# Performance work log

Hardware: AMD Instinct MI355X
Metric: run time of the kernel (lower is better)

Reference implementation:

```python
import jax, jax.numpy as jnp
import numpy as np


def setup_inputs() -> dict:
    key = jax.random.key(0)
    kx, kw = jax.random.split(key)
    x = jax.random.normal(kx, (4096, 4096), dtype=jnp.float32)
    weight = jax.random.uniform(kw, (7, 7), dtype=jnp.float32)
    bias = jnp.zeros((1,), dtype=jnp.float32)
    return {"x": x, "weight": weight, "bias": bias}


def reference(x, weight, bias):
    # Valid 2D cross-correlation (stride 1, no padding) + scalar bias,
    # identical math to corr2d(X, K) + bias in the torch module.
    lhs = x[None, None, :, :]          # [N=1, C=1, H, W]
    rhs = weight[None, None, :, :]     # [O=1, I=1, kh, kw]
    y = jax.lax.conv_general_dilated(
        lhs, rhs,
        window_strides=(1, 1),
        padding='VALID',
        dimension_numbers=('NCHW', 'OIHW', 'NCHW'),
    )
    return y[0, 0] + bias[0]  # [H-kh+1, W-kw+1]
```

## Files before the change

### kernel.cpp

```cpp
#include <hip/hip_runtime.h>

#define N   4096
#define ON  4090
#define LDS_W 136
#define CPR   34
#define WBUF  2048
#define GX  32
#define GY  512
#define NT  (GX * GY)
#define NB  (NT / 4)

__device__ __forceinline__ void gload_lds16(const float* g, float* l) {
    __builtin_amdgcn_global_load_lds(
        (const __attribute__((address_space(1))) void*)g,
        (__attribute__((address_space(3))) void*)l,
        16, 0, 0);
}

__global__ __launch_bounds__(256, 5)
void conv7x7_wave(const float* __restrict__ x,
                  const float* __restrict__ w,
                  const float* __restrict__ bias,
                  float* __restrict__ out)
{
    __shared__ float lds[4 * WBUF];

    const int tid  = threadIdx.x;
    const int lane = tid & 63;
    const int wv   = tid >> 6;
    float* buf = lds + (wv << 11);

    const int b  = blockIdx.x;
    const int bs = (b & 7) * (NB / 8) + (b >> 3);
    const int t  = (bs << 2) + wv;
    const int bx = t & (GX - 1);
    const int by = t >> 5;
    const int x0 = bx << 7;
    const int y0 = by << 3;

    {
        const int xc0 = x0 >> 2;
        #pragma unroll
        for (int k = 0; k < 8; ++k) {
            const int m   = (k << 6) + lane;
            const int row = m / CPR;
            const int cc  = m - row * CPR;
            const int gy  = min(y0 + row, N - 1);
            const int gc  = min(xc0 + cc, (N >> 2) - 1);
            const float* src = x + ((size_t)gy << 12) + ((size_t)gc << 2);
            gload_lds16(src, buf + (k << 8));
        }
    }

    float ws[49];
    #pragma unroll
    for (int i = 0; i < 49; ++i) ws[i] = w[i];
    const float bv = bias[0];

    asm volatile("s_waitcnt vmcnt(0)" ::: "memory");

    const int tau   = lane & 31;
    const int rg2   = lane >> 5;
    const int colf  = tau << 2;
    const int rbase = rg2 << 2;

    float acc[4][4] = {};

    #pragma unroll
    for (int rr = 0; rr < 10; ++rr) {
        const float* rp = buf + (rbase + rr) * LDS_W + colf;
        float v[10];
        const float4 a = *reinterpret_cast<const float4*>(rp);
        const float4 bq = *reinterpret_cast<const float4*>(rp + 4);
        const float2 c = *reinterpret_cast<const float2*>(rp + 8);
        v[0]=a.x;  v[1]=a.y;  v[2]=a.z;  v[3]=a.w;
        v[4]=bq.x; v[5]=bq.y; v[6]=bq.z; v[7]=bq.w;
        v[8]=c.x;  v[9]=c.y;

        #pragma unroll
        for (int r = 0; r < 4; ++r) {
            const int ky = rr - r;
            if (ky >= 0 && ky < 7) {
                #pragma unroll
                for (int kx = 0; kx < 7; ++kx) {
                    const float wk = ws[ky * 7 + kx];
                    #pragma unroll
                    for (int j = 0; j < 4; ++j)
                        acc[r][j] = fmaf(v[kx + j], wk, acc[r][j]);
                }
            }
        }
    }

    const int ox  = x0 + colf;
    const int oy0 = y0 + rbase;
    if (ox + 4 <= ON && oy0 + 4 <= ON) {
        #pragma unroll
        for (int r = 0; r < 4; ++r) {
            float* dst = out + (size_t)(oy0 + r) * ON + ox;
            *reinterpret_cast<float2*>(dst)     = make_float2(acc[r][0] + bv, acc[r][1] + bv);
            *reinterpret_cast<float2*>(dst + 2) = make_float2(acc[r][2] + bv, acc[r][3] + bv);
        }
    } else {
        #pragma unroll
        for (int r = 0; r < 4; ++r) {
            const int oy = oy0 + r;
            if (oy < ON) {
                float* dst = out + (size_t)oy * ON;
                #pragma unroll
                for (int j = 0; j < 4; ++j) {
                    const int oxj = ox + j;
                    if (oxj < ON) dst[oxj] = acc[r][j] + bv;
                }
            }
        }
    }
}

extern "C" void kernel_launch(void* const* d_in, const int* in_sizes, int n_in,
                              void* d_out, int out_size, void* d_ws, size_t ws_size,
                              hipStream_t stream) {
    const float* x    = (const float*)d_in[0];
    const float* w    = (const float*)d_in[1];
    const float* bias = (const float*)d_in[2];
    float* out        = (float*)d_out;

    conv7x7_wave<<<dim3(NB, 1, 1), dim3(256, 1, 1), 0, stream>>>(x, w, bias, out);
}
```

Baseline: 33.55 us.

## Double-buffer LDS staging so each wave processes four row stripes

Each wave now loops over four consecutive 8-row stripes instead of handling a single tile. It issues the async global-to-LDS load for the next stripe before computing the current one, using a partial vmcnt wait for double buffering. The grid shrinks to 1024 blocks, the launch bound drops to 2 blocks per CU, and LDS per block doubles. The aim is to hide load latency and amortise the weight loads and setup per wave, at the cost of lower occupancy and less block-level parallelism.

```diff
diff --git a/kernel.cpp b/kernel.cpp
--- a/kernel.cpp
+++ b/kernel.cpp
@@ -1,14 +1,10 @@
 #include <hip/hip_runtime.h>
 
-#define N   4096
-#define ON  4090
+#define N     4096
+#define ON    4090
 #define LDS_W 136
-#define CPR   34
-#define WBUF  2048
-#define GX  32
-#define GY  512
-#define NT  (GX * GY)
-#define NB  (NT / 4)
+#define KSTR  4
+#define NBLK  (8 * 128)
 
 __device__ __forceinline__ void gload_lds16(const float* g, float* l) {
     __builtin_amdgcn_global_load_lds(
@@ -17,100 +13,110 @@
         16, 0, 0);
 }
 
-__global__ __launch_bounds__(256, 5)
-void conv7x7_wave(const float* __restrict__ x,
+__global__ __launch_bounds__(256, 2)
+void conv7x7_pipe(const float* __restrict__ x,
                   const float* __restrict__ w,
                   const float* __restrict__ bias,
                   float* __restrict__ out)
 {
-    __shared__ float lds[4 * WBUF];
+    __shared__ float lds[4 * 4096];
 
     const int tid  = threadIdx.x;
     const int lane = tid & 63;
     const int wv   = tid >> 6;
-    float* buf = lds + (wv << 11);
 
-    const int b  = blockIdx.x;
-    const int bs = (b & 7) * (NB / 8) + (b >> 3);
-    const int t  = (bs << 2) + wv;
-    const int bx = t & (GX - 1);
-    const int by = t >> 5;
-    const int x0 = bx << 7;
-    const int y0 = by << 3;
-
-    {
-        const int xc0 = x0 >> 2;
-        #pragma unroll
-        for (int k = 0; k < 8; ++k) {
-            const int m   = (k << 6) + lane;
-            const int row = m / CPR;
-            const int cc  = m - row * CPR;
-            const int gy  = min(y0 + row, N - 1);
-            const int gc  = min(xc0 + cc, (N >> 2) - 1);
-            const float* src = x + ((size_t)gy << 12) + ((size_t)gc << 2);
-            gload_lds16(src, buf + (k << 8));
-        }
-    }
+    const int b    = blockIdx.x;
+    const int bcol = b & 7;
+    const int band = b >> 3;
+    const int x0   = ((bcol << 2) + wv) << 7;
+    const int xc0  = x0 >> 2;
+    float* buf0 = lds + (wv << 12);
 
     float ws[49];
     #pragma unroll
     for (int i = 0; i < 49; ++i) ws[i] = w[i];
     const float bv = bias[0];
 
-    asm volatile("s_waitcnt vmcnt(0)" ::: "memory");
+    auto stage = [&](float* buf, int y0) {
+        #pragma unroll
+        for (int k = 0; k < 8; ++k) {
+            const int m   = (k << 6) + lane;
+            const int row = m / 34;
+            const int cc  = m - row * 34;
+            const int gy  = min(y0 + row, N - 1);
+            const int gc  = min(xc0 + cc, (N >> 2) - 1);
+            gload_lds16(x + ((size_t)gy << 12) + ((size_t)gc << 2),
+                        buf + (k << 8));
+        }
+    };
+
+    stage(buf0, band << 5);
 
     const int tau   = lane & 31;
     const int rg2   = lane >> 5;
     const int colf  = tau << 2;
     const int rbase = rg2 << 2;
-
-    float acc[4][4] = {};
+    const int ox    = x0 + colf;
+    const bool inx  = (ox + 4 <= ON);
 
     #pragma unroll
-    for (int rr = 0; rr < 10; ++rr) {
-        const float* rp = buf + (rbase + rr) * LDS_W + colf;
-        float v[10];
-        const float4 a = *reinterpret_cast<const float4*>(rp);
-        const float4 bq = *reinterpret_cast<const float4*>(rp + 4);
-        const float2 c = *reinterpret_cast<const float2*>(rp + 8);
-        v[0]=a.x;  v[1]=a.y;  v[2]=a.z;  v[3]=a.w;
-        v[4]=bq.x; v[5]=bq.y; v[6]=bq.z; v[7]=bq.w;
-        v[8]=c.x;  v[9]=c.y;
+    for (int s = 0; s < KSTR; ++s) {
+        if (s + 1 < KSTR)
+            stage(buf0 + (((s + 1) & 1) << 11), ((band << 2) + s + 1) << 3);
 
+        if (s + 1 < KSTR) asm volatile("s_waitcnt vmcnt(8)" ::: "memory");
+        else              asm volatile("s_waitcnt vmcnt(0)" ::: "memory");
+        __builtin_amdgcn_sched_barrier(0);
+
+        const float* cbuf = buf0 + ((s & 1) << 11);
+        const int y0 = ((band << 2) + s) << 3;
+
+        float acc[4][4] = {};
         #pragma unroll
-        for (int r = 0; r < 4; ++r) {
-            const int ky = rr - r;
-            if (ky >= 0 && ky < 7) {
-                #pragma unroll
-                for (int kx = 0; kx < 7; ++kx) {
-                    const float wk = ws[ky * 7 + kx];
+        for (int rr = 0; rr < 10; ++rr) {
+            const float* rp = cbuf + (rbase + rr) * LDS_W + colf;
+            float v[10];
+            const float4 a  = *reinterpret_cast<const float4*>(rp);
+            const float4 bq = *reinterpret_cast<const float4*>(rp + 4);
+            const float2 c  = *reinterpret_cast<const float2*>(rp + 8);
+            v[0]=a.x;  v[1]=a.y;  v[2]=a.z;  v[3]=a.w;
+            v[4]=bq.x; v[5]=bq.y; v[6]=bq.z; v[7]=bq.w;
+            v[8]=c.x;  v[9]=c.y;
+
+            #pragma unroll
+            for (int r = 0; r < 4; ++r) {
+                const int ky = rr - r;
+                if (ky >= 0 && ky < 7) {
                     #pragma unroll
-                    for (int j = 0; j < 4; ++j)
-                        acc[r][j] = fmaf(v[kx + j], wk, acc[r][j]);
+                    for (int kx = 0; kx < 7; ++kx) {
+                        const float wk = ws[ky * 7 + kx];
+                        #pragma unroll
+                        for (int j = 0; j < 4; ++j)
+                            acc[r][j] = fmaf(v[kx + j], wk, acc[r][j]);
+                    }
                 }
             }
         }
-    }
 
-    const int ox  = x0 + colf;
-    const int oy0 = y0 + rbase;
-    if (ox + 4 <= ON && oy0 + 4 <= ON) {
-        #pragma unroll
-        for (int r = 0; r < 4; ++r) {
-            float* dst = out + (size_t)(oy0 + r) * ON + ox;
-            *reinterpret_cast<float2*>(dst)     = make_float2(acc[r][0] + bv, acc[r][1] + bv);
-            *reinterpret_cast<float2*>(dst + 2) = make_float2(acc[r][2] + bv, acc[r][3] + bv);
-        }
-    } else {
-        #pragma unroll
-        for (int r = 0; r < 4; ++r) {
-            const int oy = oy0 + r;
-            if (oy < ON) {
-                float* dst = out + (size_t)oy * ON;
-                #pragma unroll
-                for (int j = 0; j < 4; ++j) {
-                    const int oxj = ox + j;
-                    if (oxj < ON) dst[oxj] = acc[r][j] + bv;
+        const int oy0 = y0 + rbase;
+        if (inx && oy0 + 4 <= ON) {
+            #pragma unroll
+            for (int r = 0; r < 4; ++r) {
+                float* dst = out + (size_t)(oy0 + r) * ON + ox;
+                *reinterpret_cast<float2*>(dst)     = make_float2(acc[r][0] + bv, acc[r][1] + bv);
+                *reinterpret_cast<float2*>(dst + 2) = make_float2(acc[r][2] + bv, acc[r][3] + bv);
+            }
+        } else {
+            #pragma unroll
+            for (int r = 0; r < 4; ++r) {
+                const int oy = oy0 + r;
+                if (oy < ON) {
+                    float* dst = out + (size_t)oy * ON;
+                    #pragma unroll
+                    for (int j = 0; j < 4; ++j) {
+                        const int oxj = ox + j;
+                        if (oxj < ON) dst[oxj] = acc[r][j] + bv;
+                    }
                 }
             }
         }
@@ -125,5 +131,5 @@
     const float* bias = (const float*)d_in[2];
     float* out        = (float*)d_out;
 
-    conv7x7_wave<<<dim3(NB, 1, 1), dim3(256, 1, 1), 0, stream>>>(x, w, bias, out);
+    conv7x7_pipe<<<dim3(NBLK, 1, 1), dim3(256, 1, 1), 0, stream>>>(x, w, bias, out);
 }
```

Result: slower. 42.87 us (+27.8%).
